# Performance work log

Hardware: AMD Instinct MI355X
Metric: run time of the kernel (lower is better)

## Reference

```python
import jax, jax.numpy as jnp
import numpy as np

D_MODEL = 1024
NUM_HEADS = 16
HEAD_DIM = D_MODEL // NUM_HEADS  # 64
MAX_REL = 512
NUM_EMB = 2 * MAX_REL + 1  # 1025
B, L = 2, 2048


def _glorot(key, shape):
    fan_in, fan_out = shape[0], shape[1]
    lim = jnp.sqrt(6.0 / (fan_in + fan_out))
    return jax.random.uniform(key, shape, jnp.float32, -lim, lim)


def setup_inputs() -> dict:
    key = jax.random.key(0)
    ks = jax.random.split(key, 9)
    return {
        "query": jax.random.normal(ks[0], (B, L, D_MODEL), jnp.float32),
        "key": jax.random.normal(ks[1], (B, L, D_MODEL), jnp.float32),
        "value": jax.random.normal(ks[2], (B, L, D_MODEL), jnp.float32),
        "wq": _glorot(ks[3], (D_MODEL, D_MODEL)), "bq": jnp.zeros((D_MODEL,), jnp.float32),
        "wk": _glorot(ks[4], (D_MODEL, D_MODEL)), "bk": jnp.zeros((D_MODEL,), jnp.float32),
        "wv": _glorot(ks[5], (D_MODEL, D_MODEL)), "bv": jnp.zeros((D_MODEL,), jnp.float32),
        "wo": _glorot(ks[6], (D_MODEL, D_MODEL)), "bo": jnp.zeros((D_MODEL,), jnp.float32),
        "rel_emb": _glorot(ks[7], (NUM_EMB, HEAD_DIM)),
    }


def _split_heads(x):
    b, l, _ = x.shape
    return x.reshape(b, l, NUM_HEADS, HEAD_DIM).transpose(0, 2, 1, 3)  # (b,h,l,d)


def reference(query, key, value, wq, bq, wk, bk, wv, bv, wo, bo, rel_emb):
    q = _split_heads(query @ wq + bq)  # (b,h,l,d)
    k = _split_heads(key @ wk + bk)
    v = _split_heads(value @ wv + bv)

    # content scores: (b,h,l,l)
    content = jnp.einsum('bhid,bhjd->bhij', q, k)

    # relative position scores. Original gathers E[clip(j-i)] -> (L,L,d) then
    # einsum('bhid,ijd->bhij'). Equivalent & cheaper: project q onto all
    # relative embeddings once, then gather along the relative-index axis.
    idx = jnp.arange(q.shape[2])
    final_mat = jnp.clip(idx[None, :] - idx[:, None], -MAX_REL, MAX_REL) + MAX_REL  # (L,L)
    q_rel = jnp.einsum('bhid,rd->bhir', q, rel_emb)  # (b,h,l,num_emb)
    position = jnp.take_along_axis(q_rel, final_mat[None, None, :, :], axis=-1)  # (b,h,l,l)

    scores = (content + position) / jnp.sqrt(jnp.float32(HEAD_DIM))
    weights = jax.nn.softmax(scores, axis=-1)  # no mask, dropout off (inference)
    out = jnp.einsum('bhij,bhjd->bhid', weights, v)  # (b,h,l,d)

    out = out.transpose(0, 2, 1, 3).reshape(query.shape[0], -1, D_MODEL)
    return out @ wo + bo
```

## Files before the change

### kernel.cpp

```cpp
#include <hip/hip_runtime.h>
#include <hip/hip_bf16.h>


typedef __attribute__((ext_vector_type(8))) short short8;
typedef __attribute__((ext_vector_type(4))) float floatx4;

#define L_SEQ 2048
#define D_MODEL 1024
#define NHEAD 16
#define DH 64
#define BH 32
#define MROWS 4096

__device__ inline float b2f(short s) {
    unsigned int u = ((unsigned int)(unsigned short)s) << 16;
    float f; __builtin_memcpy(&f, &u, 4); return f;
}
__device__ inline short f2b(float f) {
    unsigned int u; __builtin_memcpy(&u, &f, 4);
    u += 0x7fffu + ((u >> 16) & 1u);
    return (short)(u >> 16);
}
__device__ inline unsigned int pack2(float a, float b) {
    __hip_bfloat162 h = __float22bfloat162_rn(make_float2(a, b));
    unsigned int u; __builtin_memcpy(&u, &h, 4); return u;
}
__device__ inline void st2(short* p, unsigned int v) {
    __builtin_memcpy(p, &v, 4);
}
__device__ inline void async_cp16(short* lds, const short* g) {
    __builtin_amdgcn_global_load_lds(
        (const __attribute__((address_space(1))) unsigned int*)g,
        (__attribute__((address_space(3))) unsigned int*)lds, 16, 0, 0);
}

__global__ __launch_bounds__(256) void detect_dtype(
        const unsigned short* __restrict__ q, int* __restrict__ flag) {
    __shared__ int s[256];
    int tid = threadIdx.x, cnt = 0;
    for (int i = tid; i < 65536; i += 256)
        if ((q[i] & 0x7F80u) == 0x7F80u) cnt++;
    s[tid] = cnt; __syncthreads();
    for (int st = 128; st; st >>= 1) {
        if (tid < st) s[tid] += s[tid + st];
        __syncthreads();
    }
    if (tid == 0) *flag = (s[0] > 4) ? 1 : 0;
}

__global__ __launch_bounds__(256) void norm_small(
        const void* __restrict__ bq, const void* __restrict__ bk,
        const void* __restrict__ bv, const void* __restrict__ bo,
        const void* __restrict__ rel, float* __restrict__ bias4,
        short* __restrict__ relb, const int* __restrict__ flagp) {
    const int f32 = *flagp;
    int t = blockIdx.x * 256 + threadIdx.x;
    if (t < 4096) {
        const void* src = (t < 1024) ? bq : (t < 2048) ? bk : (t < 3072) ? bv : bo;
        int i = t & 1023;
        bias4[t] = f32 ? ((const float*)src)[i] : b2f(((const short*)src)[i]);
    } else if (t < 4096 + 65600) {
        int i = t - 4096;
        relb[i] = f32 ? f2b(((const float*)rel)[i]) : ((const short*)rel)[i];
    }
}

__global__ __launch_bounds__(256) void transpose4(
        const void* __restrict__ w0, const void* __restrict__ w1,
        const void* __restrict__ w2, const void* __restrict__ w3,
        short* __restrict__ dst, const int* __restrict__ flagp) {
    const int f32 = *flagp;
    __shared__ short tile[32][33];
    const void* src = (blockIdx.z == 0) ? w0 : (blockIdx.z == 1) ? w1
                    : (blockIdx.z == 2) ? w2 : w3;
    short* d = dst + (size_t)blockIdx.z * (D_MODEL * D_MODEL);
    int x = blockIdx.x * 32 + threadIdx.x;
    int y0 = blockIdx.y * 32;
    for (int yy = threadIdx.y; yy < 32; yy += 8) {
        size_t idx = (size_t)(y0 + yy) * D_MODEL + x;
        tile[yy][threadIdx.x] = f32 ? f2b(((const float*)src)[idx])
                                    : ((const short*)src)[idx];
    }
    __syncthreads();
    int x0 = blockIdx.x * 32;
    for (int yy = threadIdx.y; yy < 32; yy += 8)
        d[(size_t)(x0 + yy) * D_MODEL + y0 + threadIdx.x] = tile[threadIdx.x][yy];
}

__global__ __launch_bounds__(256) void convert3(
        const float* __restrict__ q, const float* __restrict__ k,
        const float* __restrict__ v, short* __restrict__ abf_q,
        short* __restrict__ abf_k, short* __restrict__ abf_v,
        const int* __restrict__ flagp) {
    if (!*flagp) return;
    const int z = blockIdx.y;
    const float* src = (z == 0) ? q : (z == 1) ? k : v;
    short* dst = (z == 0) ? abf_q : (z == 1) ? abf_k : abf_v;
    size_t i8 = ((size_t)blockIdx.x * 256 + threadIdx.x) * 8;
    float4 f0 = *(const float4*)(&src[i8]);
    float4 f1 = *(const float4*)(&src[i8 + 4]);
    uint4 s;
    s.x = pack2(f0.x, f0.y); s.y = pack2(f0.z, f0.w);
    s.z = pack2(f1.x, f1.y); s.w = pack2(f1.z, f1.w);
    *(uint4*)(&dst[i8]) = s;
}

__global__ __launch_bounds__(256) void proj_gemm(
        const void* __restrict__ Aq, const void* __restrict__ Ak,
        const void* __restrict__ Av, const short* __restrict__ Cq,
        const short* __restrict__ Ck, const short* __restrict__ Cv,
        const short* __restrict__ WT, const float* __restrict__ bias4,
        short* __restrict__ Qout, const int* __restrict__ flagp) {
    const int f32 = *flagp;
    const int z = blockIdx.z;
    const short* A_ = f32 ? ((z == 0) ? Cq : (z == 1) ? Ck : Cv)
                          : (const short*)((z == 0) ? Aq : (z == 1) ? Ak : Av);
    const short* BT = WT + (size_t)z * (D_MODEL * D_MODEL);
    const float* bias = bias4 + z * 1024;
    short* C = Qout + (size_t)z * ((size_t)MROWS * D_MODEL);
    const int K = D_MODEL;

    __shared__ short Alds[128 * 32];
    __shared__ short Blds[128 * 32];
    const int tid = threadIdx.x;
    const int w = tid >> 6, lane = tid & 63, cl = lane & 15, quad = lane >> 4;
    const int wr = w >> 1, wc = w & 1;
    const int m0 = blockIdx.y * 128, n0 = blockIdx.x * 128;
    const int grow = lane >> 2, gcol = (lane & 3) * 8;

    floatx4 acc[4][4];
    for (int i = 0; i < 4; i++)
        for (int j = 0; j < 4; j++)
            acc[i][j] = {0.f, 0.f, 0.f, 0.f};

    for (int k0 = 0; k0 < K; k0 += 32) {
        for (int s = 0; s < 2; s++) {
            int r = w * 32 + s * 16;
            async_cp16(&Blds[r * 32], &BT[(size_t)(n0 + r + grow) * K + k0 + gcol]);
            async_cp16(&Alds[r * 32], &A_[(size_t)(m0 + r + grow) * K + k0 + gcol]);
        }
        __syncthreads();

        short8 af[4], bfr[4];
        for (int mt = 0; mt < 4; mt++)
            af[mt] = *(const short8*)(&Alds[(wr * 64 + mt * 16 + cl) * 32 + quad * 8]);
        for (int nt = 0; nt < 4; nt++)
            bfr[nt] = *(const short8*)(&Blds[(wc * 64 + nt * 16 + cl) * 32 + quad * 8]);
        for (int mt = 0; mt < 4; mt++)
            for (int nt = 0; nt < 4; nt++)
                acc[mt][nt] = __builtin_amdgcn_mfma_f32_16x16x32_bf16(
                    af[mt], bfr[nt], acc[mt][nt], 0, 0, 0);
        __syncthreads();
    }

    for (int nt = 0; nt < 4; nt++) {
        int n = n0 + wc * 64 + nt * 16 + cl;
        float bv = bias[n];
        int h = n >> 6, d = n & 63;
        for (int mt = 0; mt < 4; mt++) {
            for (int r = 0; r < 4; r++) {
                int m = m0 + wr * 64 + mt * 16 + quad * 4 + r;
                float v = acc[mt][nt][r] + bv;
                int b = m >> 11, i = m & 2047;
                if (z < 2)
                    C[(((size_t)(b * NHEAD + h)) * L_SEQ + i) * DH + d] = f2b(v);
                else
                    C[(((size_t)(b * NHEAD + h)) * DH + d) * L_SEQ + i] = f2b(v);
            }
        }
    }
}

__global__ __launch_bounds__(256) void out_gemm(
        const short* __restrict__ A, const short* __restrict__ BT,
        const float* __restrict__ bias, void* __restrict__ C_,
        const int* __restrict__ flagp) {
    const int f32 = *flagp;
    const int K = D_MODEL, N = D_MODEL;
    __shared__ short Alds[128 * 32];
    __shared__ short Blds[64 * 32];
    const int tid = threadIdx.x;
    const int w = tid >> 6, lane = tid & 63, cl = lane & 15, quad = lane >> 4;
    const int wr = w >> 1, wc = w & 1;
    const int m0 = blockIdx.y * 128, n0 = blockIdx.x * 64;
    const int grow = lane >> 2, gcol = (lane & 3) * 8;

    floatx4 acc[4][2];
    for (int i = 0; i < 4; i++)
        for (int j = 0; j < 2; j++)
            acc[i][j] = {0.f, 0.f, 0.f, 0.f};

    for (int k0 = 0; k0 < K; k0 += 32) {
        for (int s = 0; s < 2; s++) {
            int r = w * 32 + s * 16;
            async_cp16(&Alds[r * 32], &A[(size_t)(m0 + r + grow) * K + k0 + gcol]);
        }
        {
            int r = w * 16;
            async_cp16(&Blds[r * 32], &BT[(size_t)(n0 + r + grow) * K + k0 + gcol]);
        }
        __syncthreads();

        short8 af[4], bfr[2];
        for (int mt = 0; mt < 4; mt++)
            af[mt] = *(const short8*)(&Alds[(wr * 64 + mt * 16 + cl) * 32 + quad * 8]);
        for (int nt = 0; nt < 2; nt++)
            bfr[nt] = *(const short8*)(&Blds[(wc * 32 + nt * 16 + cl) * 32 + quad * 8]);
        for (int mt = 0; mt < 4; mt++)
            for (int nt = 0; nt < 2; nt++)
                acc[mt][nt] = __builtin_amdgcn_mfma_f32_16x16x32_bf16(
                    af[mt], bfr[nt], acc[mt][nt], 0, 0, 0);
        __syncthreads();
    }

    for (int nt = 0; nt < 2; nt++) {
        int n = n0 + wc * 32 + nt * 16 + cl;
        float bv = bias[n];
        for (int mt = 0; mt < 4; mt++) {
            for (int r = 0; r < 4; r++) {
                int m = m0 + wr * 64 + mt * 16 + quad * 4 + r;
                float v = acc[mt][nt][r] + bv;
                if (f32) ((float*)C_)[(size_t)m * N + n] = v;
                else     ((short*)C_)[(size_t)m * N + n] = f2b(v);
            }
        }
    }
}

__global__ __launch_bounds__(256) void attn_kernel(
        const short* __restrict__ Q, const short* __restrict__ K,
        const short* __restrict__ VT, const short* __restrict__ rel,
        short* __restrict__ out) {
    const int tid = threadIdx.x;
    const int w = tid >> 6, lane = tid & 63, cl = lane & 15, quad = lane >> 4;
    const int bh = blockIdx.y, b = bh >> 4, h = bh & 15;
    const int I0 = blockIdx.x * 64;
    const int iw0 = I0 + w * 16;

    const short* Qp = Q + (size_t)bh * L_SEQ * DH;
    const short* Kp = K + (size_t)bh * L_SEQ * DH;
    const short* Vp = VT + (size_t)bh * DH * L_SEQ;

    __shared__ short Klds[64 * 64];
    __shared__ short Vtlds[64 * 64];
    __shared__ short PpLds[4][16 * 86];
    __shared__ short Plds[4][16 * 64];

    short* PpW = &PpLds[w][0];
    short* PW  = &Plds[w][0];

    short8 aq[2];
    for (int c = 0; c < 2; c++)
        aq[c] = *(const short8*)(&Qp[(size_t)(iw0 + cl) * DH + c * 32 + quad * 8]);

    const float SCALE2 = 0.125f * 1.44269504088896340736f;
    const float FMAX = 32.0f;

    float addlo, addhi;
    {
        floatx4 Dc = {0.f, 0.f, 0.f, 0.f};
        int eidx = (cl == 1) ? 1024 : 0;
        for (int c = 0; c < 2; c++) {
            short8 ae = *(const short8*)(&rel[(size_t)eidx * DH + c * 32 + quad * 8]);
            Dc = __builtin_amdgcn_mfma_f32_16x16x32_bf16(ae, aq[c], Dc, 0, 0, 0);
        }
        float pcl = __shfl(Dc[0], cl, 64);
        float pch = __shfl(Dc[1], cl, 64);
        addlo = fmaf(pcl, SCALE2, -FMAX);
        addhi = fmaf(pch, SCALE2, -FMAX);
    }

    floatx4 O[4];
    for (int dt = 0; dt < 4; dt++) O[dt] = {0.f, 0.f, 0.f, 0.f};
    float lsum = 0.f;

    const int srow = tid >> 2;
    const int spair = (tid & 3) * 2;

    for (int j0 = 0; j0 < L_SEQ; j0 += 64) {
        for (int s = 0; s < 2; s++) {
            int chunk = spair + s;
            int pos = chunk ^ (srow & 7);
            *(short8*)(&Klds[srow * 64 + pos * 8]) =
                *(const short8*)(&Kp[(size_t)(j0 + srow) * DH + chunk * 8]);
            *(short8*)(&Vtlds[srow * 64 + pos * 8]) =
                *(const short8*)(&Vp[(size_t)srow * L_SEQ + j0 + chunk * 8]);
        }
        __syncthreads();

        const bool hi_clamp = (j0 - iw0 - 15) >= 512;
        const bool lo_clamp = (j0 + 63 - iw0) <= -512;
        const bool banded = !(hi_clamp || lo_clamp);
        const float addc = hi_clamp ? addhi : addlo;

        floatx4 St[4];
        for (int jt = 0; jt < 4; jt++) {
            St[jt] = {0.f, 0.f, 0.f, 0.f};
            int row = jt * 16 + cl;
            for (int c = 0; c < 2; c++) {
                int pos = ((4 * c + quad) ^ (cl & 7)) * 8;
                short8 bk = *(const short8*)(&Klds[row * 64 + pos]);
                St[jt] = __builtin_amdgcn_mfma_f32_16x16x32_bf16(bk, aq[c], St[jt], 0, 0, 0);
            }
        }

        if (banded) {
            floatx4 Pt[5];
            for (int pt = 0; pt < 5; pt++) Pt[pt] = {0.f, 0.f, 0.f, 0.f};
            const int base = j0 - iw0 - 15;
            for (int pt = 0; pt < 5; pt++) {
                int raw = pt * 16 + cl + base;
                int idx = (raw < -512 ? -512 : (raw > 512 ? 512 : raw)) + 512;
                const short* ep = rel + (size_t)idx * DH;
                for (int c = 0; c < 2; c++) {
                    short8 be = *(const short8*)(&ep[c * 32 + quad * 8]);
                    Pt[pt] = __builtin_amdgcn_mfma_f32_16x16x32_bf16(be, aq[c], Pt[pt], 0, 0, 0);
                }
            }
            for (int pt = 0; pt < 5; pt++) {
                int t = pt * 16 + quad * 4;
                st2(&PpW[cl * 86 + t],     pack2(Pt[pt][0], Pt[pt][1]));
                st2(&PpW[cl * 86 + t + 2], pack2(Pt[pt][2], Pt[pt][3]));
            }
            for (int jt = 0; jt < 4; jt++)
                for (int r = 0; r < 4; r++) {
                    int t = jt * 16 + quad * 4 + r - cl + 15;
                    float pos = b2f(PpW[cl * 86 + t]);
                    St[jt][r] = fmaf(St[jt][r], SCALE2, fmaf(pos, SCALE2, -FMAX));
                }
        } else {
            for (int jt = 0; jt < 4; jt++)
                for (int r = 0; r < 4; r++)
                    St[jt][r] = fmaf(St[jt][r], SCALE2, addc);
        }

        for (int jt = 0; jt < 4; jt++)
            for (int r = 0; r < 4; r++) {
                float p = __builtin_amdgcn_exp2f(St[jt][r]);
                St[jt][r] = p;
                lsum += p;
            }

        for (int jt = 0; jt < 4; jt++)
            for (int pr = 0; pr < 2; pr++) {
                int jl = jt * 16 + quad * 4 + pr * 2;
                int addr = cl * 64 + ((jl >> 3) ^ (cl & 7)) * 8 + (jl & 7);
                st2(&PW[addr], pack2(St[jt][2 * pr], St[jt][2 * pr + 1]));
            }

        for (int c = 0; c < 2; c++) {
            int ppos = ((4 * c + quad) ^ (cl & 7)) * 8;
            short8 bp = *(const short8*)(&PW[cl * 64 + ppos]);
            for (int dt = 0; dt < 4; dt++) {
                int row = dt * 16 + cl;
                int vpos = ((4 * c + quad) ^ (cl & 7)) * 8;
                short8 av = *(const short8*)(&Vtlds[row * 64 + vpos]);
                O[dt] = __builtin_amdgcn_mfma_f32_16x16x32_bf16(av, bp, O[dt], 0, 0, 0);
            }
        }
        __syncthreads();
    }

    lsum += __shfl_xor(lsum, 16, 64);
    lsum += __shfl_xor(lsum, 32, 64);
    float inv = 1.0f / lsum;

    for (int dt = 0; dt < 4; dt++)
        for (int pr = 0; pr < 2; pr++) {
            int jl = dt * 16 + quad * 4 + pr * 2;
            int addr = cl * 64 + ((jl >> 3) ^ (cl & 7)) * 8 + (jl & 7);
            st2(&PW[addr], pack2(O[dt][2 * pr] * inv, O[dt][2 * pr + 1] * inv));
        }
    size_t obase = ((size_t)b * L_SEQ + iw0 + cl) * D_MODEL + h * DH;
    for (int s = 0; s < 2; s++) {
        int c2 = quad * 2 + s;
        short8 o = *(const short8*)(&PW[cl * 64 + (c2 ^ (cl & 7)) * 8]);
        *(short8*)(&out[obase + c2 * 8]) = o;
    }
}

extern "C" void kernel_launch(void* const* d_in, const int* in_sizes, int n_in,
                              void* d_out, int out_size, void* d_ws, size_t ws_size,
                              hipStream_t stream) {
    const void* query = d_in[0];
    const void* key   = d_in[1];
    const void* value = d_in[2];
    const void* wq = d_in[3];  const void* bq = d_in[4];
    const void* wk = d_in[5];  const void* bk = d_in[6];
    const void* wv = d_in[7];  const void* bv = d_in[8];
    const void* wo = d_in[9];  const void* bo = d_in[10];
    const void* rel = d_in[11];

    int* flag = (int*)d_ws;
    short* ws = (short*)d_ws + 16;
    const size_t WSZ = (size_t)D_MODEL * D_MODEL;
    const size_t TSZ = (size_t)MROWS * D_MODEL;
    short* WT   = ws;
    short* Qw   = ws + 4 * WSZ;
    short* Kw   = Qw + TSZ;
    short* Vtw  = Kw + TSZ;
    short* Attw = Vtw + TSZ;
    float* bias4 = (float*)(Attw + TSZ);
    short* relb  = (short*)(bias4 + 4096);

    short* Cq = (short*)d_out;
    short* Ck = (short*)d_out + TSZ;
    short* Cv = Attw;

    detect_dtype<<<1, 256, 0, stream>>>((const unsigned short*)query, flag);
    norm_small<<<273, 256, 0, stream>>>(bq, bk, bv, bo, rel, bias4, relb, flag);
    transpose4<<<dim3(32, 32, 4), dim3(32, 8), 0, stream>>>(wq, wk, wv, wo, WT, flag);

    convert3<<<dim3(2048, 3), 256, 0, stream>>>(
        (const float*)query, (const float*)key, (const float*)value,
        Cq, Ck, Cv, flag);

    proj_gemm<<<dim3(8, 32, 3), 256, 0, stream>>>(query, key, value,
                                                  Cq, Ck, Cv, WT, bias4,
                                                  Qw, flag);

    attn_kernel<<<dim3(L_SEQ / 64, BH), 256, 0, stream>>>(Qw, Kw, Vtw, relb, Attw);

    out_gemm<<<dim3(16, 32), 256, 0, stream>>>(Attw, WT + 3 * WSZ, bias4 + 3072,
                                               d_out, flag);
}
```

Measured before the change: 382.1 us.

## Double-buffer K/V tiles with async global-to-LDS prefetch in attention loop

Replaces the synchronous per-iteration K and V^T tile loads into shared memory with a two-buffer scheme. The next tile is fetched asynchronously with async_cp16 while the current tile is used for the score, softmax and PV MFMAs. One barrier per iteration replaces the previous two. This aims to hide global-memory latency behind compute, at the cost of doubling the K/V LDS footprint, which may reduce occupancy.

```diff
diff --git a/kernel.cpp b/kernel.cpp
--- a/kernel.cpp
+++ b/kernel.cpp
@@ -241,8 +241,8 @@
     const short* Kp = K + (size_t)bh * L_SEQ * DH;
     const short* Vp = VT + (size_t)bh * DH * L_SEQ;
 
-    __shared__ short Klds[64 * 64];
-    __shared__ short Vtlds[64 * 64];
+    __shared__ short Klds2[2][64 * 64];
+    __shared__ short Vtlds2[2][64 * 64];
     __shared__ short PpLds[4][16 * 86];
     __shared__ short Plds[4][16 * 64];
 
@@ -274,19 +274,32 @@
     for (int dt = 0; dt < 4; dt++) O[dt] = {0.f, 0.f, 0.f, 0.f};
     float lsum = 0.f;
 
-    const int srow = tid >> 2;
-    const int spair = (tid & 3) * 2;
+    const int lr = lane >> 3;
+    const int lc8 = ((lane & 7) ^ lr) * 8;
+
+    for (int s = 0; s < 2; s++) {
+        int g = w * 2 + s;
+        int r = g * 8 + lr;
+        async_cp16(&Klds2[0][g * 512], &Kp[(size_t)r * DH + lc8]);
+        async_cp16(&Vtlds2[0][g * 512], &Vp[(size_t)r * L_SEQ + lc8]);
+    }
+    int cur = 0;
 
     for (int j0 = 0; j0 < L_SEQ; j0 += 64) {
-        for (int s = 0; s < 2; s++) {
-            int chunk = spair + s;
-            int pos = chunk ^ (srow & 7);
-            *(short8*)(&Klds[srow * 64 + pos * 8]) =
-                *(const short8*)(&Kp[(size_t)(j0 + srow) * DH + chunk * 8]);
-            *(short8*)(&Vtlds[srow * 64 + pos * 8]) =
-                *(const short8*)(&Vp[(size_t)srow * L_SEQ + j0 + chunk * 8]);
-        }
-        __syncthreads();
+        __syncthreads();
+
+        if (j0 + 64 < L_SEQ) {
+            for (int s = 0; s < 2; s++) {
+                int g = w * 2 + s;
+                int r = g * 8 + lr;
+                async_cp16(&Klds2[cur ^ 1][g * 512],
+                           &Kp[(size_t)(j0 + 64 + r) * DH + lc8]);
+                async_cp16(&Vtlds2[cur ^ 1][g * 512],
+                           &Vp[(size_t)r * L_SEQ + (j0 + 64) + lc8]);
+            }
+        }
+        const short* Kb = &Klds2[cur][0];
+        const short* Vb = &Vtlds2[cur][0];
 
         const bool hi_clamp = (j0 - iw0 - 15) >= 512;
         const bool lo_clamp = (j0 + 63 - iw0) <= -512;
@@ -299,7 +312,7 @@
             int row = jt * 16 + cl;
             for (int c = 0; c < 2; c++) {
                 int pos = ((4 * c + quad) ^ (cl & 7)) * 8;
-                short8 bk = *(const short8*)(&Klds[row * 64 + pos]);
+                short8 bk = *(const short8*)(&Kb[row * 64 + pos]);
                 St[jt] = __builtin_amdgcn_mfma_f32_16x16x32_bf16(bk, aq[c], St[jt], 0, 0, 0);
             }
         }
@@ -354,11 +367,11 @@
             for (int dt = 0; dt < 4; dt++) {
                 int row = dt * 16 + cl;
                 int vpos = ((4 * c + quad) ^ (cl & 7)) * 8;
-                short8 av = *(const short8*)(&Vtlds[row * 64 + vpos]);
+                short8 av = *(const short8*)(&Vb[row * 64 + vpos]);
                 O[dt] = __builtin_amdgcn_mfma_f32_16x16x32_bf16(av, bp, O[dt], 0, 0, 0);
             }
         }
-        __syncthreads();
+        cur ^= 1;
     }
 
     lsum += __shfl_xor(lsum, 16, 64);
```

After: 409.4 us. 7.1% more time.
